# Kernel optimization log

Hardware: AMD Instinct MI355X
Metric: run time of the kernel (lower is better)

## Reference

```python
import jax, jax.numpy as jnp
import numpy as np
from jax import lax


def _combine(proj):
    # proj: [B,2,4,4]; returns 4x4 with top 3 rows = K[:3,:3] @ E[:3,:4]
    E = proj[:, 0]
    Km = proj[:, 1, :3, :3]
    top = jnp.einsum('bij,bjk->bik', Km, E[:, :3, :4])
    return jnp.concatenate([top, E[:, 3:4, :]], axis=1)


def _bilinear_sample(img, ix, iy):
    # img [B,C,H,W]; ix,iy [B,P] pixel coords (align_corners=True), zero padding
    B, C, H, W = img.shape
    x0 = jnp.floor(ix); y0 = jnp.floor(iy)
    x1 = x0 + 1.0; y1 = y0 + 1.0
    wx1 = ix - x0; wx0 = 1.0 - wx1
    wy1 = iy - y0; wy0 = 1.0 - wy1
    flat = img.reshape(B, C, H * W)
    def gather(xf, yf):
        valid = (xf >= 0) & (xf <= W - 1) & (yf >= 0) & (yf <= H - 1)
        xi = jnp.clip(xf, 0, W - 1).astype(jnp.int32)
        yi = jnp.clip(yf, 0, H - 1).astype(jnp.int32)
        idx = (yi * W + xi)[:, None, :]               # [B,1,P]
        v = jnp.take_along_axis(flat, idx, axis=2)    # [B,C,P]
        return v * valid[:, None, :].astype(img.dtype)
    return (gather(x0, y0) * (wx0 * wy0)[:, None, :]
          + gather(x1, y0) * (wx1 * wy0)[:, None, :]
          + gather(x0, y1) * (wx0 * wy1)[:, None, :]
          + gather(x1, y1) * (wx1 * wy1)[:, None, :])


def _homo_warp(src_fea, src_proj, ref_proj, depth_values):
    # MVSNet differentiable homography warping
    B, C, H, W = src_fea.shape
    D = depth_values.shape[1]
    proj = jnp.einsum('bij,bjk->bik', src_proj, jnp.linalg.inv(ref_proj))
    rot = proj[:, :3, :3]; trans = proj[:, :3, 3]
    yy, xx = jnp.meshgrid(jnp.arange(H, dtype=src_fea.dtype),
                          jnp.arange(W, dtype=src_fea.dtype), indexing='ij')
    xyz = jnp.stack([xx.ravel(), yy.ravel(), jnp.ones(H * W, src_fea.dtype)])  # [3,HW]
    rot_xyz = jnp.einsum('bij,jp->bip', rot, xyz)                              # [B,3,HW]
    pts = rot_xyz[:, :, None, :] * depth_values[:, None, :, None] \
        + trans[:, :, None, None]                                              # [B,3,D,HW]
    ix = (pts[:, 0] / pts[:, 2]).reshape(B, -1)
    iy = (pts[:, 1] / pts[:, 2]).reshape(B, -1)
    return _bilinear_sample(src_fea, ix, iy).reshape(B, C, D, H, W)


def _forward(features, proj_matrices, depth_values, w_reg, num_depth):
    B, V, C, H, W = features.shape
    D = num_depth
    ref_proj = _combine(proj_matrices[:, 0])
    ref_vol = jnp.broadcast_to(features[:, 0][:, :, None], (B, C, D, H, W))
    vol_sum = ref_vol
    vol_sq = ref_vol ** 2
    for v in range(1, V):  # fixed small number of views
        src_proj = _combine(proj_matrices[:, v])
        w = _homo_warp(features[:, v], src_proj, ref_proj, depth_values)
        vol_sum = vol_sum + w
        vol_sq = vol_sq + w ** 2
    variance = vol_sq / V - (vol_sum / V) ** 2
    # stand-in cost_regularization: single 3D conv C->1, k=3, SAME
    cost = lax.conv_general_dilated(variance, w_reg, (1, 1, 1), 'SAME',
                                    dimension_numbers=('NCDHW', 'OIDHW', 'NCDHW'))[:, 0]
    prob = jax.nn.softmax(cost, axis=1)
    # prev_state branch: is_begin is all-True (video start) -> warped_costvol == 0
    # (original then L1-normalizes prob_volume, overwriting itg_prob_volume)
    itg = prob / jnp.maximum(jnp.sum(jnp.abs(prob), axis=1, keepdims=True), 1e-12)
    depth = jnp.sum(itg * depth_values[:, :, None, None], axis=1)
    # photometric confidence (no_grad in original)
    padded = jnp.pad(prob, ((0, 0), (1, 2), (0, 0), (0, 0)))
    sum4 = lax.reduce_window(padded, 0.0, lax.add, (1, 4, 1, 1), (1, 1, 1, 1), 'VALID')
    di = jnp.sum(prob * jnp.arange(D, dtype=prob.dtype)[None, :, None, None], axis=1)
    di = jnp.clip(di.astype(jnp.int32), 0, D - 1)
    conf = jnp.take_along_axis(sum4, di[:, None], axis=1)[:, 0]
    return depth, conf, itg


def setup_inputs() -> dict:
    key = jax.random.key(0)
    k1, k2 = jax.random.split(key)
    B, V, C, D, H, W = 2, 5, 32, 48, 128, 160
    features = jax.random.normal(k1, (B, V, C, H, W), jnp.float32)
    f = 200.0
    K = np.eye(4, dtype=np.float32)
    K[0, 0] = f; K[1, 1] = f; K[0, 2] = W / 2.0; K[1, 2] = H / 2.0
    projs = []
    for v in range(V):
        E = np.eye(4, dtype=np.float32)
        E[0, 3] = 0.1 * v  # small camera baseline per view
        projs.append(np.stack([E, K]))
    proj_matrices = jnp.asarray(np.tile(np.stack(projs)[None], (B, 1, 1, 1, 1)))
    depth_values = jnp.tile(jnp.linspace(425.0, 935.0, D, dtype=jnp.float32)[None], (B, 1))
    w_reg = jax.random.normal(k2, (1, C, 3, 3, 3), jnp.float32) * 0.05
    is_begin = jnp.ones((B,), bool)
    return dict(features=features, proj_matrices=proj_matrices,
                depth_values=depth_values, w_reg=w_reg, is_begin=is_begin,
                num_depth=D, stage_idx=0)


def reference(features, proj_matrices, depth_values, w_reg, is_begin, num_depth, stage_idx):
    return _forward(features, proj_matrices, depth_values, w_reg, num_depth)
```

## Files before the change

### kernel.cpp

```cpp
#include <hip/hip_runtime.h>
#include <math.h>

constexpr int B_ = 2;
constexpr int V_ = 5;
constexpr int C_ = 32;
constexpr int D_ = 48;
constexpr int H_ = 128;
constexpr int W_ = 160;
constexpr int HW_ = H_ * W_;
constexpr int NVOX = B_ * D_ * HW_;
constexpr int PLANE = D_ * HW_;

typedef short short8 __attribute__((ext_vector_type(8)));
typedef float floatx4 __attribute__((ext_vector_type(4)));


__device__ inline void combine4(const float* pm, float out[4][4]) {
    const float* E = pm;
    const float* K = pm + 16;
    for (int i = 0; i < 3; ++i)
        for (int j = 0; j < 4; ++j) {
            float a = 0.f;
            for (int k = 0; k < 3; ++k) a += K[i * 4 + k] * E[k * 4 + j];
            out[i][j] = a;
        }
    for (int j = 0; j < 4; ++j) out[3][j] = E[12 + j];
}

__device__ inline void invert4(const float A[4][4], float inv[4][4]) {
    float M[4][8];
    for (int i = 0; i < 4; ++i)
        for (int j = 0; j < 4; ++j) {
            M[i][j] = A[i][j];
            M[i][4 + j] = (i == j) ? 1.f : 0.f;
        }
    for (int col = 0; col < 4; ++col) {
        int piv = col;
        float best = fabsf(M[col][col]);
        for (int r = col + 1; r < 4; ++r) {
            float v = fabsf(M[r][col]);
            if (v > best) { best = v; piv = r; }
        }
        if (piv != col)
            for (int j = 0; j < 8; ++j) { float t = M[col][j]; M[col][j] = M[piv][j]; M[piv][j] = t; }
        float ip = 1.f / M[col][col];
        for (int j = 0; j < 8; ++j) M[col][j] *= ip;
        for (int r = 0; r < 4; ++r) {
            if (r == col) continue;
            float f = M[r][col];
            for (int j = 0; j < 8; ++j) M[r][j] -= f * M[col][j];
        }
    }
    for (int i = 0; i < 4; ++i)
        for (int j = 0; j < 4; ++j) inv[i][j] = M[i][4 + j];
}

__device__ inline unsigned bf_rne(float f) {
    unsigned u = __float_as_uint(f);
    return (u + 0x7FFFu + ((u >> 16) & 1u)) >> 16;
}

__device__ inline float bflo(unsigned u) { return __uint_as_float(u << 16); }
__device__ inline float bfhi(unsigned u) { return __uint_as_float(u & 0xffff0000u); }

__global__ void setup_kernel(const float* __restrict__ proj, const float* __restrict__ wreg,
                             float* __restrict__ rt, unsigned* __restrict__ wtb) {
    int t = threadIdx.x;
    if (t < B_) {
        int b = t;
        float ref[4][4], inv[4][4];
        combine4(proj + (size_t)((b * V_ + 0) * 2) * 16, ref);
        invert4(ref, inv);
        for (int v = 1; v < V_; ++v) {
            float src[4][4];
            combine4(proj + (size_t)((b * V_ + v) * 2) * 16, src);
            float P[3][4];
            for (int i = 0; i < 3; ++i)
                for (int j = 0; j < 4; ++j) {
                    float a = 0.f;
                    for (int k = 0; k < 4; ++k) a += src[i][k] * inv[k][j];
                    P[i][j] = a;
                }
            float* o = rt + (size_t)(b * (V_ - 1) + (v - 1)) * 12;
            o[0] = P[0][0]; o[1] = P[0][1]; o[2] = P[0][2];
            o[3] = P[1][0]; o[4] = P[1][1]; o[5] = P[1][2];
            o[6] = P[2][0]; o[7] = P[2][1]; o[8] = P[2][2];
            o[9] = P[0][3]; o[10] = P[1][3]; o[11] = P[2][3];
        }
    }
    if (t < 128) {
        int i = t >> 6;
        int lane = t & 63;
        int q = lane >> 4;
        int l = lane & 15;
        int tap = i * 16 + l;
        unsigned u[4];
#pragma unroll
        for (int jj = 0; jj < 4; ++jj) {
            int ch0 = q * 8 + 2 * jj;
            float v0 = (tap < 27) ? wreg[ch0 * 27 + tap] : 0.f;
            float v1 = (tap < 27) ? wreg[(ch0 + 1) * 27 + tap] : 0.f;
            u[jj] = bf_rne(v0) | (bf_rne(v1) << 16);
        }
        uint4* o = (uint4*)wtb;
        o[i * 64 + lane] = make_uint4(u[0], u[1], u[2], u[3]);
    }
}

__global__ __launch_bounds__(256) void transpose_kernel(const float* __restrict__ feat,
                                                        unsigned* __restrict__ feat_cl) {
    int idx = blockIdx.x * 256 + threadIdx.x;
    if (idx >= B_ * V_ * HW_) return;
    int pix = idx % HW_;
    int bv = idx / HW_;
    const float* src = feat + (size_t)bv * C_ * HW_ + pix;
    unsigned u[16];
#pragma unroll
    for (int j = 0; j < 16; ++j) {
        float a = src[(size_t)(2 * j) * HW_];
        float b = src[(size_t)(2 * j + 1) * HW_];
        u[j] = bf_rne(a) | (bf_rne(b) << 16);
    }
    uint4* dst = (uint4*)(feat_cl + (size_t)idx * 16);
    dst[0] = make_uint4(u[0], u[1], u[2], u[3]);
    dst[1] = make_uint4(u[4], u[5], u[6], u[7]);
    dst[2] = make_uint4(u[8], u[9], u[10], u[11]);
    dst[3] = make_uint4(u[12], u[13], u[14], u[15]);
}

__global__ __launch_bounds__(256) void warp_kernel(const unsigned char* __restrict__ fb,
                                                   const float* __restrict__ rt,
                                                   const float* __restrict__ dv,
                                                   const unsigned* __restrict__ wtb,
                                                   unsigned short* __restrict__ T) {
    const int tid = threadIdx.x;
    const int lane = tid & 63;
    const int cq = tid & 3;
    const int b = blockIdx.z;
    const int d = blockIdx.y;
    const int pixb = blockIdx.x * 64;
    const int pix = pixb + (tid >> 2);
    const int w = pix % W_;
    const int h = pix / W_;
    const float wf = (float)w, hf = (float)h;
    const float dep = dv[b * D_ + d];

    const uint4* wp = (const uint4*)wtb;
    uint4 a0u = wp[lane];
    uint4 a1u = wp[64 + lane];

    float w00, w01, w10, w11;
    int pix00, pix01, pix10, pix11;
    {
        const float* m = rt + (b * (V_ - 1) + cq) * 12;
        float xp = fmaf(fmaf(m[0], wf, fmaf(m[1], hf, m[2])), dep, m[9]);
        float yp = fmaf(fmaf(m[3], wf, fmaf(m[4], hf, m[5])), dep, m[10]);
        float zp = fmaf(fmaf(m[6], wf, fmaf(m[7], hf, m[8])), dep, m[11]);
        float iz = __builtin_amdgcn_rcpf(zp);
        float ix = xp * iz, iy = yp * iz;
        float x0f = floorf(ix), y0f = floorf(iy);
        float wx1 = ix - x0f, wx0 = 1.f - wx1;
        float wy1 = iy - y0f, wy0 = 1.f - wy1;
        float x1f = x0f + 1.f, y1f = y0f + 1.f;
        bool vx0 = (x0f >= 0.f) && (x0f <= (float)(W_ - 1));
        bool vx1 = (x1f >= 0.f) && (x1f <= (float)(W_ - 1));
        bool vy0 = (y0f >= 0.f) && (y0f <= (float)(H_ - 1));
        bool vy1 = (y1f >= 0.f) && (y1f <= (float)(H_ - 1));
        int x0i = (int)fminf(fmaxf(x0f, 0.f), (float)(W_ - 1));
        int x1i = (int)fminf(fmaxf(x1f, 0.f), (float)(W_ - 1));
        int y0i = (int)fminf(fmaxf(y0f, 0.f), (float)(H_ - 1));
        int y1i = (int)fminf(fmaxf(y1f, 0.f), (float)(H_ - 1));
        w00 = wx0 * wy0 * ((vx0 && vy0) ? 1.f : 0.f);
        w01 = wx1 * wy0 * ((vx1 && vy0) ? 1.f : 0.f);
        w10 = wx0 * wy1 * ((vx0 && vy1) ? 1.f : 0.f);
        w11 = wx1 * wy1 * ((vx1 && vy1) ? 1.f : 0.f);
        pix00 = y0i * W_ + x0i;
        pix01 = y0i * W_ + x1i;
        pix10 = y1i * W_ + x0i;
        pix11 = y1i * W_ + x1i;
    }

    float s[8], q[8];
    {
        const unsigned char* rb = fb + (size_t)(b * V_) * HW_ * 64;
        uint4 r = *(const uint4*)(rb + (((unsigned)pix) << 6) + (cq << 4));
        float f0 = bflo(r.x), f1 = bfhi(r.x);
        float f2 = bflo(r.y), f3 = bfhi(r.y);
        float f4 = bflo(r.z), f5 = bfhi(r.z);
        float f6 = bflo(r.w), f7 = bfhi(r.w);
        s[0] = f0; s[1] = f1; s[2] = f2; s[3] = f3;
        s[4] = f4; s[5] = f5; s[6] = f6; s[7] = f7;
        q[0] = f0 * f0; q[1] = f1 * f1; q[2] = f2 * f2; q[3] = f3 * f3;
        q[4] = f4 * f4; q[5] = f5 * f5; q[6] = f6 * f6; q[7] = f7 * f7;
    }

#pragma unroll
    for (int v = 0; v < V_ - 1; ++v) {
        int sl = (lane & ~3) | v;
        float W00 = __shfl(w00, sl), W01 = __shfl(w01, sl);
        float W10 = __shfl(w10, sl), W11 = __shfl(w11, sl);
        unsigned O00 = ((unsigned)__shfl(pix00, sl) << 6) + (cq << 4);
        unsigned O01 = ((unsigned)__shfl(pix01, sl) << 6) + (cq << 4);
        unsigned O10 = ((unsigned)__shfl(pix10, sl) << 6) + (cq << 4);
        unsigned O11 = ((unsigned)__shfl(pix11, sl) << 6) + (cq << 4);
        const unsigned char* base = fb + (size_t)(b * V_ + v + 1) * HW_ * 64;
        uint4 c0 = *(const uint4*)(base + O00);
        uint4 c1 = *(const uint4*)(base + O01);
        uint4 c2 = *(const uint4*)(base + O10);
        uint4 c3 = *(const uint4*)(base + O11);
        unsigned u0[4] = {c0.x, c0.y, c0.z, c0.w};
        unsigned u1[4] = {c1.x, c1.y, c1.z, c1.w};
        unsigned u2[4] = {c2.x, c2.y, c2.z, c2.w};
        unsigned u3[4] = {c3.x, c3.y, c3.z, c3.w};
#pragma unroll
        for (int jj = 0; jj < 4; ++jj) {
            float a0 = bflo(u0[jj]);
            float b0 = bflo(u1[jj]);
            float g0 = bflo(u2[jj]);
            float d0 = bflo(u3[jj]);
            float acc = fmaf(a0, W00, fmaf(b0, W01, fmaf(g0, W10, d0 * W11)));
            s[2 * jj] += acc;
            q[2 * jj] = fmaf(acc, acc, q[2 * jj]);
            float a1 = bfhi(u0[jj]);
            float b1 = bfhi(u1[jj]);
            float g1 = bfhi(u2[jj]);
            float d1 = bfhi(u3[jj]);
            float acc1 = fmaf(a1, W00, fmaf(b1, W01, fmaf(g1, W10, d1 * W11)));
            s[2 * jj + 1] += acc1;
            q[2 * jj + 1] = fmaf(acc1, acc1, q[2 * jj + 1]);
        }
    }

    const float invV = 1.0f / (float)V_;
    unsigned pk[4];
#pragma unroll
    for (int jj = 0; jj < 4; ++jj) {
        float m0 = s[2 * jj] * invV, m1 = s[2 * jj + 1] * invV;
        float v0 = fmaf(-m0, m0, q[2 * jj] * invV);
        float v1 = fmaf(-m1, m1, q[2 * jj + 1] * invV);
        pk[jj] = bf_rne(v0) | (bf_rne(v1) << 16);
    }

    uint4 bu;
    {
        int srcl = ((lane & 15) << 2) + (lane >> 4);
        bu.x = (unsigned)__shfl((int)pk[0], srcl);
        bu.y = (unsigned)__shfl((int)pk[1], srcl);
        bu.z = (unsigned)__shfl((int)pk[2], srcl);
        bu.w = (unsigned)__shfl((int)pk[3], srcl);
    }
    short8 bfrag = __builtin_bit_cast(short8, bu);
    short8 afrag0 = __builtin_bit_cast(short8, a0u);
    short8 afrag1 = __builtin_bit_cast(short8, a1u);

    floatx4 z = {0.f, 0.f, 0.f, 0.f};
    floatx4 t0 = __builtin_amdgcn_mfma_f32_16x16x32_bf16(afrag0, bfrag, z, 0, 0, 0);
    floatx4 t1 = __builtin_amdgcn_mfma_f32_16x16x32_bf16(afrag1, bfrag, z, 0, 0, 0);

    const unsigned gidx = (unsigned)(b * PLANE + d * HW_ + pixb + ((tid >> 6) << 4) + (lane & 15));
    const int tq = (lane >> 4) << 2;
#pragma unroll
    for (int r = 0; r < 4; ++r) {
        T[(unsigned)((tq + r) * NVOX) + gidx] = (unsigned short)bf_rne(t0[r]);
        int tap2 = 16 + tq + r;
        if (tap2 < 27) T[(unsigned)(tap2 * NVOX) + gidx] = (unsigned short)bf_rne(t1[r]);
    }
}

__global__ __launch_bounds__(256) void cost_kernel(const unsigned short* __restrict__ T,
                                                   float* __restrict__ cost) {
    int t = blockIdx.x * 256 + threadIdx.x;
    int v0 = t * 8;
    int w0 = v0 % W_;
    int h = (v0 / W_) % H_;
    int d = (v0 / HW_) % D_;
    int b = v0 / PLANE;
    float acc[8];
#pragma unroll
    for (int i = 0; i < 8; ++i) acc[i] = 0.f;

#pragma unroll
    for (int kd = 0; kd < 3; ++kd) {
        int dd = d + kd - 1;
        if (dd < 0 || dd >= D_) continue;
#pragma unroll
        for (int kh = 0; kh < 3; ++kh) {
            int hh = h + kh - 1;
            if (hh < 0 || hh >= H_) continue;
            unsigned r = (unsigned)(b * PLANE + dd * HW_ + hh * W_);
            int j = kd * 9 + kh * 3;
            const unsigned short* p0 = T + (size_t)j * NVOX + r;
            const unsigned short* p1 = p0 + NVOX;
            const unsigned short* p2 = p1 + NVOX;
            uint4 A0 = *(const uint4*)(p0 + w0);
            uint4 A1 = *(const uint4*)(p1 + w0);
            uint4 A2 = *(const uint4*)(p2 + w0);
            float eL = (w0 > 0) ? bflo((unsigned)p0[w0 - 1]) : 0.f;
            float eR = (w0 + 8 < W_) ? bflo((unsigned)p2[w0 + 8]) : 0.f;
            unsigned x0[4] = {A0.x, A0.y, A0.z, A0.w};
            unsigned x1[4] = {A1.x, A1.y, A1.z, A1.w};
            unsigned x2[4] = {A2.x, A2.y, A2.z, A2.w};
            float a0[8], a1[8], a2[8];
#pragma unroll
            for (int k = 0; k < 4; ++k) {
                a0[2 * k] = bflo(x0[k]); a0[2 * k + 1] = bfhi(x0[k]);
                a1[2 * k] = bflo(x1[k]); a1[2 * k + 1] = bfhi(x1[k]);
                a2[2 * k] = bflo(x2[k]); a2[2 * k + 1] = bfhi(x2[k]);
            }
            acc[0] += eL + a1[0] + a2[1];
#pragma unroll
            for (int i = 1; i < 7; ++i) acc[i] += a0[i - 1] + a1[i] + a2[i + 1];
            acc[7] += a0[6] + a1[7] + eR;
        }
    }
    float4* cp = (float4*)(cost + v0);
    cp[0] = make_float4(acc[0], acc[1], acc[2], acc[3]);
    cp[1] = make_float4(acc[4], acc[5], acc[6], acc[7]);
}

__global__ __launch_bounds__(256) void out_kernel(const float* __restrict__ cost,
                                                  const float* __restrict__ dv,
                                                  float* __restrict__ out) {
    __shared__ float red[4][64];
    const int tid = threadIdx.x;
    const int lane = tid & 63;
    const int wq = tid >> 6;
    const int pixg = blockIdx.x * 64 + lane;
    const int b = pixg / HW_;
    const int pix = pixg - b * HW_;
    const float* cb = cost + (size_t)b * PLANE + pix;

    float p[12];
    float mx = -1e30f;
#pragma unroll
    for (int i = 0; i < 12; ++i) {
        p[i] = cb[(size_t)(wq * 12 + i) * HW_];
        mx = fmaxf(mx, p[i]);
    }
    red[wq][lane] = mx;
    __syncthreads();
    mx = fmaxf(fmaxf(red[0][lane], red[1][lane]), fmaxf(red[2][lane], red[3][lane]));
    float S = 0.f;
#pragma unroll
    for (int i = 0; i < 12; ++i) {
        p[i] = expf(p[i] - mx);
        S += p[i];
    }
    __syncthreads();
    red[wq][lane] = S;
    __syncthreads();
    S = red[0][lane] + red[1][lane] + red[2][lane] + red[3][lane];
    float invS = 1.f / S;
    float S2p = 0.f;
#pragma unroll
    for (int i = 0; i < 12; ++i) {
        p[i] *= invS;
        S2p += p[i];
    }
    __syncthreads();
    red[wq][lane] = S2p;
    __syncthreads();
    float S2 = red[0][lane] + red[1][lane] + red[2][lane] + red[3][lane];
    float invS2 = 1.f / fmaxf(S2, 1e-12f);
    float dp = 0.f, difp = 0.f;
#pragma unroll
    for (int i = 0; i < 12; ++i) {
        int d0 = wq * 12 + i;
        dp = fmaf(p[i] * invS2, dv[b * D_ + d0], dp);
        difp = fmaf(p[i], (float)d0, difp);
    }
    __syncthreads();
    red[wq][lane] = dp;
    __syncthreads();
    float depth = red[0][lane] + red[1][lane] + red[2][lane] + red[3][lane];
    __syncthreads();
    red[wq][lane] = difp;
    __syncthreads();
    float dif = red[0][lane] + red[1][lane] + red[2][lane] + red[3][lane];
    int di = (int)dif;
    di = min(max(di, 0), D_ - 1);
    float cf = 0.f;
#pragma unroll
    for (int i = 0; i < 12; ++i) {
        int d0 = wq * 12 + i;
        if (d0 >= di - 1 && d0 <= di + 2) cf += p[i];
    }
    __syncthreads();
    red[wq][lane] = cf;
    __syncthreads();
    float conf = red[0][lane] + red[1][lane] + red[2][lane] + red[3][lane];

    if (wq == 0) {
        out[pixg] = depth;
        out[B_ * HW_ + pixg] = conf;
    }
    float* itg = out + 2 * B_ * HW_ + (size_t)b * PLANE + pix;
#pragma unroll
    for (int i = 0; i < 12; ++i)
        itg[(size_t)(wq * 12 + i) * HW_] = p[i] * invS2;
}

extern "C" void kernel_launch(void* const* d_in, const int* in_sizes, int n_in,
                              void* d_out, int out_size, void* d_ws, size_t ws_size,
                              hipStream_t stream) {
    const float* feat = (const float*)d_in[0];
    const float* proj = (const float*)d_in[1];
    const float* dv   = (const float*)d_in[2];
    const float* wreg = (const float*)d_in[3];
    float* out = (float*)d_out;
    float* ws = (float*)d_ws;

    const size_t rt_off = 0;
    const size_t rt_sz = 128;
    const size_t wtb_off = rt_off + rt_sz;
    const size_t wtb_sz = 512;
    const size_t fcl_off = wtb_off + wtb_sz;
    const size_t fcl_sz = (size_t)B_ * V_ * HW_ * 16;
    const size_t T_off = fcl_off + fcl_sz;
    const size_t T_sz = (size_t)27 * NVOX / 2;
    const size_t cost_off = T_off + T_sz;
    const size_t cost_sz = (size_t)NVOX;
    const size_t need = (cost_off + cost_sz) * sizeof(float);
    if (ws_size < need) return;

    float* rt = ws + rt_off;
    unsigned* wtb = (unsigned*)(ws + wtb_off);
    unsigned* feat_cl = (unsigned*)(ws + fcl_off);
    unsigned short* T = (unsigned short*)(ws + T_off);
    float* cost = ws + cost_off;

    setup_kernel<<<1, 128, 0, stream>>>(proj, wreg, rt, wtb);
    transpose_kernel<<<(B_ * V_ * HW_) / 256, 256, 0, stream>>>(feat, feat_cl);
    dim3 wgrid(HW_ / 64, D_, B_);
    warp_kernel<<<wgrid, 256, 0, stream>>>((const unsigned char*)feat_cl, rt, dv, wtb, T);
    cost_kernel<<<(NVOX / 8) / 256, 256, 0, stream>>>(T, cost);
    out_kernel<<<(B_ * HW_) / 64, 256, 0, stream>>>(cost, dv, out);
}
```

Before: 217.7 us.

## Fuse cost aggregation and softmax/output kernels via shared-memory cost tile

Merges the 3D stencil cost kernel and the per-pixel softmax/depth regression kernel into one kernel. Each 384-thread block computes the full 48-depth cost column for 64 pixels into LDS, then performs the depth reductions from shared memory. This removes the fp32 cost volume write and read through global memory plus one launch, at the cost of a smaller grid (640 blocks) and larger blocks with 6-way reductions.

Measured after the change: 221.7 us. Within noise of the previous version (+1.8%).

```diff
diff --git a/kernel.cpp b/kernel.cpp
--- a/kernel.cpp
+++ b/kernel.cpp
@@ -267,137 +267,140 @@
     }
 }
 
-__global__ __launch_bounds__(256) void cost_kernel(const unsigned short* __restrict__ T,
-                                                   float* __restrict__ cost) {
-    int t = blockIdx.x * 256 + threadIdx.x;
-    int v0 = t * 8;
-    int w0 = v0 % W_;
-    int h = (v0 / W_) % H_;
-    int d = (v0 / HW_) % D_;
-    int b = v0 / PLANE;
-    float acc[8];
-#pragma unroll
-    for (int i = 0; i < 8; ++i) acc[i] = 0.f;
-
-#pragma unroll
-    for (int kd = 0; kd < 3; ++kd) {
-        int dd = d + kd - 1;
-        if (dd < 0 || dd >= D_) continue;
-#pragma unroll
-        for (int kh = 0; kh < 3; ++kh) {
-            int hh = h + kh - 1;
-            if (hh < 0 || hh >= H_) continue;
-            unsigned r = (unsigned)(b * PLANE + dd * HW_ + hh * W_);
-            int j = kd * 9 + kh * 3;
-            const unsigned short* p0 = T + (size_t)j * NVOX + r;
-            const unsigned short* p1 = p0 + NVOX;
-            const unsigned short* p2 = p1 + NVOX;
-            uint4 A0 = *(const uint4*)(p0 + w0);
-            uint4 A1 = *(const uint4*)(p1 + w0);
-            uint4 A2 = *(const uint4*)(p2 + w0);
-            float eL = (w0 > 0) ? bflo((unsigned)p0[w0 - 1]) : 0.f;
-            float eR = (w0 + 8 < W_) ? bflo((unsigned)p2[w0 + 8]) : 0.f;
-            unsigned x0[4] = {A0.x, A0.y, A0.z, A0.w};
-            unsigned x1[4] = {A1.x, A1.y, A1.z, A1.w};
-            unsigned x2[4] = {A2.x, A2.y, A2.z, A2.w};
-            float a0[8], a1[8], a2[8];
-#pragma unroll
-            for (int k = 0; k < 4; ++k) {
-                a0[2 * k] = bflo(x0[k]); a0[2 * k + 1] = bfhi(x0[k]);
-                a1[2 * k] = bflo(x1[k]); a1[2 * k + 1] = bfhi(x1[k]);
-                a2[2 * k] = bflo(x2[k]); a2[2 * k + 1] = bfhi(x2[k]);
+__global__ __launch_bounds__(384) void costout_kernel(const unsigned short* __restrict__ T,
+                                                      const float* __restrict__ dv,
+                                                      float* __restrict__ out) {
+    __shared__ float lc[D_][64];
+    __shared__ float red[6][64];
+    const int tid = threadIdx.x;
+    const int pix0 = blockIdx.x * 64;
+
+    {
+        const int o = tid & 7;
+        const int d = tid >> 3;
+        const int pg = pix0 + o * 8;
+        const int b = pg / HW_;
+        const int pp = pg - b * HW_;
+        const int h = pp / W_;
+        const int w0 = pp - h * W_;
+        float acc[8];
+#pragma unroll
+        for (int i = 0; i < 8; ++i) acc[i] = 0.f;
+#pragma unroll
+        for (int kd = 0; kd < 3; ++kd) {
+            int dd = d + kd - 1;
+            if (dd < 0 || dd >= D_) continue;
+#pragma unroll
+            for (int kh = 0; kh < 3; ++kh) {
+                int hh = h + kh - 1;
+                if (hh < 0 || hh >= H_) continue;
+                unsigned r = (unsigned)(b * PLANE + dd * HW_ + hh * W_);
+                int j = kd * 9 + kh * 3;
+                const unsigned short* p0 = T + (size_t)j * NVOX + r;
+                const unsigned short* p1 = p0 + NVOX;
+                const unsigned short* p2 = p1 + NVOX;
+                uint4 A0 = *(const uint4*)(p0 + w0);
+                uint4 A1 = *(const uint4*)(p1 + w0);
+                uint4 A2 = *(const uint4*)(p2 + w0);
+                float eL = (w0 > 0) ? bflo((unsigned)p0[w0 - 1]) : 0.f;
+                float eR = (w0 + 8 < W_) ? bflo((unsigned)p2[w0 + 8]) : 0.f;
+                unsigned x0[4] = {A0.x, A0.y, A0.z, A0.w};
+                unsigned x1[4] = {A1.x, A1.y, A1.z, A1.w};
+                unsigned x2[4] = {A2.x, A2.y, A2.z, A2.w};
+                float a0[8], a1[8], a2[8];
+#pragma unroll
+                for (int k = 0; k < 4; ++k) {
+                    a0[2 * k] = bflo(x0[k]); a0[2 * k + 1] = bfhi(x0[k]);
+                    a1[2 * k] = bflo(x1[k]); a1[2 * k + 1] = bfhi(x1[k]);
+                    a2[2 * k] = bflo(x2[k]); a2[2 * k + 1] = bfhi(x2[k]);
+                }
+                acc[0] += eL + a1[0] + a2[1];
+#pragma unroll
+                for (int i = 1; i < 7; ++i) acc[i] += a0[i - 1] + a1[i] + a2[i + 1];
+                acc[7] += a0[6] + a1[7] + eR;
             }
-            acc[0] += eL + a1[0] + a2[1];
-#pragma unroll
-            for (int i = 1; i < 7; ++i) acc[i] += a0[i - 1] + a1[i] + a2[i + 1];
-            acc[7] += a0[6] + a1[7] + eR;
-        }
-    }
-    float4* cp = (float4*)(cost + v0);
-    cp[0] = make_float4(acc[0], acc[1], acc[2], acc[3]);
-    cp[1] = make_float4(acc[4], acc[5], acc[6], acc[7]);
-}
-
-__global__ __launch_bounds__(256) void out_kernel(const float* __restrict__ cost,
-                                                  const float* __restrict__ dv,
-                                                  float* __restrict__ out) {
-    __shared__ float red[4][64];
-    const int tid = threadIdx.x;
-    const int lane = tid & 63;
-    const int wq = tid >> 6;
-    const int pixg = blockIdx.x * 64 + lane;
+        }
+#pragma unroll
+        for (int i = 0; i < 8; ++i) lc[d][o * 8 + i] = acc[i];
+    }
+    __syncthreads();
+
+    const int l = tid & 63;
+    const int g = tid / 64;
+    const int pixg = pix0 + l;
     const int b = pixg / HW_;
-    const int pix = pixg - b * HW_;
-    const float* cb = cost + (size_t)b * PLANE + pix;
-
-    float p[12];
+    const int pp = pixg - b * HW_;
+
+    float p[8];
     float mx = -1e30f;
 #pragma unroll
-    for (int i = 0; i < 12; ++i) {
-        p[i] = cb[(size_t)(wq * 12 + i) * HW_];
+    for (int i = 0; i < 8; ++i) {
+        p[i] = lc[g * 8 + i][l];
         mx = fmaxf(mx, p[i]);
     }
-    red[wq][lane] = mx;
-    __syncthreads();
-    mx = fmaxf(fmaxf(red[0][lane], red[1][lane]), fmaxf(red[2][lane], red[3][lane]));
+    red[g][l] = mx;
+    __syncthreads();
+    mx = red[0][l];
+#pragma unroll
+    for (int k = 1; k < 6; ++k) mx = fmaxf(mx, red[k][l]);
     float S = 0.f;
 #pragma unroll
-    for (int i = 0; i < 12; ++i) {
+    for (int i = 0; i < 8; ++i) {
         p[i] = expf(p[i] - mx);
         S += p[i];
     }
     __syncthreads();
-    red[wq][lane] = S;
-    __syncthreads();
-    S = red[0][lane] + red[1][lane] + red[2][lane] + red[3][lane];
+    red[g][l] = S;
+    __syncthreads();
+    S = red[0][l] + red[1][l] + red[2][l] + red[3][l] + red[4][l] + red[5][l];
     float invS = 1.f / S;
     float S2p = 0.f;
 #pragma unroll
-    for (int i = 0; i < 12; ++i) {
+    for (int i = 0; i < 8; ++i) {
         p[i] *= invS;
         S2p += p[i];
     }
     __syncthreads();
-    red[wq][lane] = S2p;
-    __syncthreads();
-    float S2 = red[0][lane] + red[1][lane] + red[2][lane] + red[3][lane];
+    red[g][l] = S2p;
+    __syncthreads();
+    float S2 = red[0][l] + red[1][l] + red[2][l] + red[3][l] + red[4][l] + red[5][l];
     float invS2 = 1.f / fmaxf(S2, 1e-12f);
     float dp = 0.f, difp = 0.f;
 #pragma unroll
-    for (int i = 0; i < 12; ++i) {
-        int d0 = wq * 12 + i;
+    for (int i = 0; i < 8; ++i) {
+        int d0 = g * 8 + i;
         dp = fmaf(p[i] * invS2, dv[b * D_ + d0], dp);
         difp = fmaf(p[i], (float)d0, difp);
     }
     __syncthreads();
-    red[wq][lane] = dp;
-    __syncthreads();
-    float depth = red[0][lane] + red[1][lane] + red[2][lane] + red[3][lane];
-    __syncthreads();
-    red[wq][lane] = difp;
-    __syncthreads();
-    float dif = red[0][lane] + red[1][lane] + red[2][lane] + red[3][lane];
+    red[g][l] = dp;
+    __syncthreads();
+    float depth = red[0][l] + red[1][l] + red[2][l] + red[3][l] + red[4][l] + red[5][l];
+    __syncthreads();
+    red[g][l] = difp;
+    __syncthreads();
+    float dif = red[0][l] + red[1][l] + red[2][l] + red[3][l] + red[4][l] + red[5][l];
     int di = (int)dif;
     di = min(max(di, 0), D_ - 1);
     float cf = 0.f;
 #pragma unroll
-    for (int i = 0; i < 12; ++i) {
-        int d0 = wq * 12 + i;
+    for (int i = 0; i < 8; ++i) {
+        int d0 = g * 8 + i;
         if (d0 >= di - 1 && d0 <= di + 2) cf += p[i];
     }
     __syncthreads();
-    red[wq][lane] = cf;
-    __syncthreads();
-    float conf = red[0][lane] + red[1][lane] + red[2][lane] + red[3][lane];
-
-    if (wq == 0) {
+    red[g][l] = cf;
+    __syncthreads();
+    float conf = red[0][l] + red[1][l] + red[2][l] + red[3][l] + red[4][l] + red[5][l];
+
+    if (g == 0) {
         out[pixg] = depth;
         out[B_ * HW_ + pixg] = conf;
     }
-    float* itg = out + 2 * B_ * HW_ + (size_t)b * PLANE + pix;
-#pragma unroll
-    for (int i = 0; i < 12; ++i)
-        itg[(size_t)(wq * 12 + i) * HW_] = p[i] * invS2;
+    float* itg = out + 2 * B_ * HW_ + (size_t)b * PLANE + pp;
+#pragma unroll
+    for (int i = 0; i < 8; ++i)
+        itg[(size_t)(g * 8 + i) * HW_] = p[i] * invS2;
 }
 
 extern "C" void kernel_launch(void* const* d_in, const int* in_sizes, int n_in,
@@ -418,21 +421,17 @@
     const size_t fcl_sz = (size_t)B_ * V_ * HW_ * 16;
     const size_t T_off = fcl_off + fcl_sz;
     const size_t T_sz = (size_t)27 * NVOX / 2;
-    const size_t cost_off = T_off + T_sz;
-    const size_t cost_sz = (size_t)NVOX;
-    const size_t need = (cost_off + cost_sz) * sizeof(float);
+    const size_t need = (T_off + T_sz) * sizeof(float);
     if (ws_size < need) return;
 
     float* rt = ws + rt_off;
     unsigned* wtb = (unsigned*)(ws + wtb_off);
     unsigned* feat_cl = (unsigned*)(ws + fcl_off);
     unsigned short* T = (unsigned short*)(ws + T_off);
-    float* cost = ws + cost_off;
 
     setup_kernel<<<1, 128, 0, stream>>>(proj, wreg, rt, wtb);
     transpose_kernel<<<(B_ * V_ * HW_) / 256, 256, 0, stream>>>(feat, feat_cl);
     dim3 wgrid(HW_ / 64, D_, B_);
     warp_kernel<<<wgrid, 256, 0, stream>>>((const unsigned char*)feat_cl, rt, dv, wtb, T);
-    cost_kernel<<<(NVOX / 8) / 256, 256, 0, stream>>>(T, cost);
-    out_kernel<<<(B_ * HW_) / 64, 256, 0, stream>>>(cost, dv, out);
-}
+    costout_kernel<<<(B_ * HW_) / 64, 384, 0, stream>>>(T, dv, out);
+}
```
